# Optimization experiments

Measured on AMD Instinct MI355X. Metric: run time of the kernel, lower is better.

Reference implementation:

```python
import jax, jax.numpy as jnp
import numpy as np

N = 8192
DELTA_DELAY = 1.0
T_REFRACTORY = 2.0
RESET_POTENTIAL = 0.0


def setup_inputs() -> dict:
    key = jax.random.key(0)
    k_w, k_i = jax.random.split(key)
    ones = jnp.ones((N,), jnp.float32)
    return {
        "I_ext": jax.random.normal(k_i, (N,), jnp.float32),
        "w": jnp.clip(0.5 * jax.random.normal(k_w, (N, N), jnp.float32), -10.0, 10.0),
        "v": jnp.zeros((N,), jnp.float32),              # v = E_L = 0
        "spiked": jnp.zeros((N,), jnp.float32),
        "time_since_spike": 10000.0 * ones,
        "theta_v": 15.0 * ones,                          # theta_inf
        "tau_m": 10.0 * ones,
        "tau_s": 4.0 * ones,
        "tau_theta": 1000.0 * ones,
        "J_theta": 1.0 * ones,
        "E_L": jnp.zeros((N,), jnp.float32),
        "c": 0.1 * ones,
        "Delta_u": 5.0 * ones,
        "theta_inf": 15.0 * ones,
    }


def reference(I_ext, w, v, spiked, time_since_spike, theta_v,
              tau_m, tau_s, tau_theta, J_theta, E_L, c, Delta_u, theta_inf):
    # adaptation threshold update
    theta_v = theta_v + (theta_inf - theta_v + J_theta * spiked) / tau_theta
    # synaptic pulse kernel (elementwise over neurons)
    t = time_since_spike - DELTA_DELAY
    eps = (1.0 + jnp.tanh(t)) * jnp.exp(-t / tau_s) / tau_s
    # mask out self-recurrence, then matvec: [N,N] @ [N] -> [N]
    W_syn = w * (1.0 - jnp.eye(w.shape[0], dtype=w.dtype))
    I_syn = W_syn @ eps
    # membrane potential update
    v_next = v + (E_L - v + I_ext) / tau_m + I_syn
    not_refractory = jnp.where(time_since_spike > T_REFRACTORY, 1.0, 0.0)
    spikes_lambda = jnp.clip(not_refractory * c * jnp.exp((v_next - theta_v) / Delta_u), 0.0, 1.0)
    # Bernoulli spike sampling (fixed key for reproducibility)
    spiked_new = jax.random.bernoulli(jax.random.key(42), spikes_lambda).astype(spikes_lambda.dtype)
    not_spiked = 1.0 - spiked_new
    v_new = not_spiked * v_next + spiked_new * RESET_POTENTIAL
    return spikes_lambda, spiked_new, v_new
```

## Files before the change

### kernel.cpp

```cpp
#include <hip/hip_runtime.h>
#include <stdint.h>

__device__ __forceinline__ unsigned int rotl32(unsigned int x, unsigned int d) {
    return (x << d) | (x >> (32u - d));
}

__device__ __forceinline__ void threefry2x32_key0_42(unsigned int c0, unsigned int c1,
                                                     unsigned int& o0, unsigned int& o1) {
    const unsigned int ks0 = 0u;
    const unsigned int ks1 = 42u;
    const unsigned int ks2 = 0x1BD11BDAu ^ 0u ^ 42u;
    unsigned int x0 = c0 + ks0;
    unsigned int x1 = c1 + ks1;
#define TF_RND(r) { x0 += x1; x1 = rotl32(x1, (r)); x1 ^= x0; }
    TF_RND(13) TF_RND(15) TF_RND(26) TF_RND(6)
    x0 += ks1; x1 += ks2 + 1u;
    TF_RND(17) TF_RND(29) TF_RND(16) TF_RND(24)
    x0 += ks2; x1 += ks0 + 2u;
    TF_RND(13) TF_RND(15) TF_RND(26) TF_RND(6)
    x0 += ks0; x1 += ks1 + 3u;
    TF_RND(17) TF_RND(29) TF_RND(16) TF_RND(24)
    x0 += ks1; x1 += ks2 + 4u;
    TF_RND(13) TF_RND(15) TF_RND(26) TF_RND(6)
    x0 += ks2; x1 += ks0 + 5u;
#undef TF_RND
    o0 = x0; o1 = x1;
}

__device__ __forceinline__ float jax_uniform_u01(unsigned int n) {
    unsigned int o0, o1;
    threefry2x32_key0_42(0u, n, o0, o1);
    unsigned int bits = o0 ^ o1;
    unsigned int fb = (bits >> 9) | 0x3F800000u;
    float u = __uint_as_float(fb) - 1.0f;
    return fmaxf(u, 0.0f);
}

__global__ void eps_kernel(const float* __restrict__ tss,
                           const float* __restrict__ tau_s,
                           float* __restrict__ eps, int N) {
    int i = blockIdx.x * blockDim.x + threadIdx.x;
    if (i < N) {
        float t  = tss[i] - 1.0f;
        float ts = tau_s[i];
        eps[i] = (1.0f + tanhf(t)) * expf(-t / ts) / ts;
    }
}

__global__ __launch_bounds__(256) void row_update_kernel(
    const float* __restrict__ w,
    const float* __restrict__ eps,
    const float* __restrict__ I_ext,
    const float* __restrict__ v,
    const float* __restrict__ spiked,
    const float* __restrict__ tss,
    const float* __restrict__ theta_v,
    const float* __restrict__ tau_m,
    const float* __restrict__ tau_theta,
    const float* __restrict__ J_theta,
    const float* __restrict__ E_L,
    const float* __restrict__ c,
    const float* __restrict__ Delta_u,
    const float* __restrict__ theta_inf,
    float* __restrict__ out, int N) {

    const int row = blockIdx.x;
    const int tid = threadIdx.x;
    const float4* __restrict__ wrow = (const float4*)(w + (size_t)row * (size_t)N);
    const float4* __restrict__ e4   = (const float4*)eps;

    float acc = 0.0f;
    const int n4 = N >> 2;
    for (int idx = tid; idx < n4; idx += 256) {
        float4 wv = wrow[idx];
        float4 ev = e4[idx];
        acc += wv.x * ev.x + wv.y * ev.y + wv.z * ev.z + wv.w * ev.w;
    }

    #pragma unroll
    for (int off = 32; off > 0; off >>= 1)
        acc += __shfl_down(acc, off, 64);

    __shared__ float wsum[4];
    const int wid  = tid >> 6;
    const int lane = tid & 63;
    if (lane == 0) wsum[wid] = acc;
    __syncthreads();

    if (tid == 0) {
        float I_syn = wsum[0] + wsum[1] + wsum[2] + wsum[3];
        I_syn -= w[(size_t)row * (size_t)N + row] * eps[row];

        float th = theta_v[row] +
                   (theta_inf[row] - theta_v[row] + J_theta[row] * spiked[row]) / tau_theta[row];
        float v_next = v[row] + (E_L[row] - v[row] + I_ext[row]) / tau_m[row] + I_syn;

        float notref = (tss[row] > 2.0f) ? 1.0f : 0.0f;
        float lam = notref * c[row] * expf((v_next - th) / Delta_u[row]);
        lam = fminf(fmaxf(lam, 0.0f), 1.0f);

        float u = jax_uniform_u01((unsigned int)row);
        float s = (u < lam) ? 1.0f : 0.0f;
        float v_new = (1.0f - s) * v_next;

        out[row]         = lam;
        out[N + row]     = s;
        out[2 * N + row] = v_new;
    }
}

extern "C" void kernel_launch(void* const* d_in, const int* in_sizes, int n_in,
                              void* d_out, int out_size, void* d_ws, size_t ws_size,
                              hipStream_t stream) {
    const int N = in_sizes[0];
    const float* I_ext     = (const float*)d_in[0];
    const float* w         = (const float*)d_in[1];
    const float* v         = (const float*)d_in[2];
    const float* spiked    = (const float*)d_in[3];
    const float* tss       = (const float*)d_in[4];
    const float* theta_v   = (const float*)d_in[5];
    const float* tau_m     = (const float*)d_in[6];
    const float* tau_s     = (const float*)d_in[7];
    const float* tau_theta = (const float*)d_in[8];
    const float* J_theta   = (const float*)d_in[9];
    const float* E_L       = (const float*)d_in[10];
    const float* c         = (const float*)d_in[11];
    const float* Delta_u   = (const float*)d_in[12];
    const float* theta_inf = (const float*)d_in[13];
    float* out = (float*)d_out;
    float* eps = (float*)d_ws;

    hipLaunchKernelGGL(eps_kernel, dim3((N + 255) / 256), dim3(256), 0, stream,
                       tss, tau_s, eps, N);
    hipLaunchKernelGGL(row_update_kernel, dim3(N), dim3(256), 0, stream,
                       w, eps, I_ext, v, spiked, tss, theta_v, tau_m, tau_theta,
                       J_theta, E_L, c, Delta_u, theta_inf, out, N);
}
```

Before: 382.8 us.

## Map one wavefront per matrix row and unroll matvec with independent accumulators

Each 64-lane wavefront now computes a full row dot product, and a block covers four rows, so the shared-memory reduction and block barrier go away. The inner loop is unrolled four ways, issuing four float4 loads of w and eps before any accumulation, with separate FMA accumulators to raise memory-level parallelism. Each wave now streams a whole 32KB row by itself and the grid shrinks by a factor of four.

```diff
diff --git a/kernel.cpp b/kernel.cpp
--- a/kernel.cpp
+++ b/kernel.cpp
@@ -64,32 +64,44 @@
     const float* __restrict__ theta_inf,
     float* __restrict__ out, int N) {
 
-    const int row = blockIdx.x;
-    const int tid = threadIdx.x;
+    const int wid  = threadIdx.x >> 6;
+    const int lane = threadIdx.x & 63;
+    const int row  = blockIdx.x * 4 + wid;
+    if (row >= N) return;
+
     const float4* __restrict__ wrow = (const float4*)(w + (size_t)row * (size_t)N);
     const float4* __restrict__ e4   = (const float4*)eps;
+    const int n4 = N >> 2;
 
-    float acc = 0.0f;
-    const int n4 = N >> 2;
-    for (int idx = tid; idx < n4; idx += 256) {
+    float a0 = 0.0f, a1 = 0.0f, a2 = 0.0f, a3 = 0.0f;
+    int idx = lane;
+    for (; idx + 192 < n4; idx += 256) {
+        float4 w0 = wrow[idx];
+        float4 w1 = wrow[idx + 64];
+        float4 w2 = wrow[idx + 128];
+        float4 w3 = wrow[idx + 192];
+        float4 e0 = e4[idx];
+        float4 e1 = e4[idx + 64];
+        float4 e2 = e4[idx + 128];
+        float4 e3 = e4[idx + 192];
+        a0 = fmaf(w0.x, e0.x, fmaf(w0.y, e0.y, fmaf(w0.z, e0.z, fmaf(w0.w, e0.w, a0))));
+        a1 = fmaf(w1.x, e1.x, fmaf(w1.y, e1.y, fmaf(w1.z, e1.z, fmaf(w1.w, e1.w, a1))));
+        a2 = fmaf(w2.x, e2.x, fmaf(w2.y, e2.y, fmaf(w2.z, e2.z, fmaf(w2.w, e2.w, a2))));
+        a3 = fmaf(w3.x, e3.x, fmaf(w3.y, e3.y, fmaf(w3.z, e3.z, fmaf(w3.w, e3.w, a3))));
+    }
+    for (; idx < n4; idx += 64) {
         float4 wv = wrow[idx];
         float4 ev = e4[idx];
-        acc += wv.x * ev.x + wv.y * ev.y + wv.z * ev.z + wv.w * ev.w;
+        a0 = fmaf(wv.x, ev.x, fmaf(wv.y, ev.y, fmaf(wv.z, ev.z, fmaf(wv.w, ev.w, a0))));
     }
+    float acc = (a0 + a1) + (a2 + a3);
 
     #pragma unroll
     for (int off = 32; off > 0; off >>= 1)
         acc += __shfl_down(acc, off, 64);
 
-    __shared__ float wsum[4];
-    const int wid  = tid >> 6;
-    const int lane = tid & 63;
-    if (lane == 0) wsum[wid] = acc;
-    __syncthreads();
-
-    if (tid == 0) {
-        float I_syn = wsum[0] + wsum[1] + wsum[2] + wsum[3];
-        I_syn -= w[(size_t)row * (size_t)N + row] * eps[row];
+    if (lane == 0) {
+        float I_syn = acc - w[(size_t)row * (size_t)N + row] * eps[row];
 
         float th = theta_v[row] +
                    (theta_inf[row] - theta_v[row] + J_theta[row] * spiked[row]) / tau_theta[row];
@@ -132,7 +144,7 @@
 
     hipLaunchKernelGGL(eps_kernel, dim3((N + 255) / 256), dim3(256), 0, stream,
                        tss, tau_s, eps, N);
-    hipLaunchKernelGGL(row_update_kernel, dim3(N), dim3(256), 0, stream,
+    hipLaunchKernelGGL(row_update_kernel, dim3((N + 3) / 4), dim3(256), 0, stream,
                        w, eps, I_ext, v, spiked, tss, theta_v, tau_m, tau_theta,
                        J_theta, E_L, c, Delta_u, theta_inf, out, N);
 }
```

Result: no change. 381.2 us (-0.4%).
